# Optimization experiments

Hardware: AMD Instinct MI355X
Metric: run time of the kernel (lower is better)

Reference implementation:

```python
import jax, jax.numpy as jnp
import numpy as np

D_MODEL = 512
N_HEADS = 8
HEAD_SIZE = 64


def setup_inputs() -> dict:
    key = jax.random.key(0)
    ks = jax.random.split(key, 6)
    B, T = 4, 2048
    x_q = jax.random.normal(ks[0], (B, T, D_MODEL), dtype=jnp.float32)
    s = 1.0 / np.sqrt(D_MODEL)
    # per-head q/k/v projection weights, stacked: [H, head_size, d_model]
    Wq = jax.random.normal(ks[1], (N_HEADS, HEAD_SIZE, D_MODEL), dtype=jnp.float32) * s
    Wk = jax.random.normal(ks[2], (N_HEADS, HEAD_SIZE, D_MODEL), dtype=jnp.float32) * s
    Wv = jax.random.normal(ks[3], (N_HEADS, HEAD_SIZE, D_MODEL), dtype=jnp.float32) * s
    Wp = jax.random.normal(ks[4], (D_MODEL, D_MODEL), dtype=jnp.float32) * s
    bp = jax.random.normal(ks[5], (D_MODEL,), dtype=jnp.float32) * 0.01
    return {"x_q": x_q, "Wq": Wq, "Wk": Wk, "Wv": Wv, "Wp": Wp, "bp": bp}


def reference(x_q, Wq, Wk, Wv, Wp, bp):
    B, T, C = x_q.shape  # C == d_model
    # per-head projections: [B, H, T, K]
    q = jnp.einsum('btd,hkd->bhtk', x_q, Wq)
    k = jnp.einsum('btd,hkd->bhtk', x_q, Wk)
    v = jnp.einsum('btd,hkd->bhtk', x_q, Wv)
    # NOTE: original scales by C**-0.5 with C = d_model (not head_size)
    scores = jnp.einsum('bhtk,bhsk->bhts', q, k) * (C ** -0.5)
    causal = jnp.tril(jnp.ones((T, T), dtype=bool))
    scores = jnp.where(causal, scores, -jnp.inf)
    wei = jax.nn.softmax(scores, axis=-1)  # dropout is identity in eval
    out = jnp.einsum('bhts,bhsk->bhtk', wei, v)
    # concat heads: [B, T, H*K] == [B, T, d_model]
    out = out.transpose(0, 2, 1, 3).reshape(B, T, C)
    return out @ Wp.T + bp
```

## Files before the change

kernel.cpp:

```cpp
#include <hip/hip_runtime.h>
#include <hip/hip_bf16.h>

using bf16x8 = __attribute__((ext_vector_type(8))) __bf16;
using f32x4  = __attribute__((ext_vector_type(4))) float;
using f32x16 = __attribute__((ext_vector_type(16))) float;
using i32x4  = __attribute__((ext_vector_type(4))) int;

#define MFMA_16x16x32(a, b, c) __builtin_amdgcn_mfma_f32_16x16x32_bf16((a), (b), (c), 0, 0, 0)
#define MFMA32(a, b, c)        __builtin_amdgcn_mfma_f32_32x32x16_bf16((a), (b), (c), 0, 0, 0)

#define GLOAD16(g, l)                                                         \
    __builtin_amdgcn_global_load_lds(                                         \
        (const __attribute__((address_space(1))) unsigned int*)(g),           \
        (__attribute__((address_space(3))) unsigned int*)(l), 16, 0, 0)

__device__ __forceinline__ ushort f2bf(float f) {
    return __builtin_bit_cast(ushort, (__bf16)f);
}
__device__ __forceinline__ unsigned pk_bf16(float lo, float hi) {
    unsigned r;
    asm volatile("v_cvt_pk_bf16_f32 %0, %1, %2" : "=v"(r) : "v"(lo), "v"(hi));
    return r;
}
__device__ __forceinline__ void pl32_swap(unsigned &a, unsigned &b) {
    asm volatile("v_permlane32_swap_b32 %0, %1" : "+v"(a), "+v"(b));
}

__global__ __launch_bounds__(256) void cvt_bf16(
    const float* __restrict__ in, ushort* __restrict__ out, int n)
{
    const int i = (blockIdx.x * 256 + threadIdx.x) * 8;
    if (i + 8 <= n) {
        const f32x4 a = *(const f32x4*)(in + i);
        const f32x4 b = *(const f32x4*)(in + i + 4);
        union { ushort u[8]; i32x4 w; } p;
        #pragma unroll
        for (int j = 0; j < 4; ++j) { p.u[j] = f2bf(a[j]); p.u[4 + j] = f2bf(b[j]); }
        *(i32x4*)(out + i) = p.w;
    }
}

__global__ __launch_bounds__(256) void cvt_w3(
    const float* __restrict__ w0, const float* __restrict__ w1,
    const float* __restrict__ w2, ushort* __restrict__ out)
{
    const int i = (blockIdx.x * 256 + threadIdx.x) * 8;
    const int w = i >> 18, off = i & 262143;
    const float* src = (w == 0) ? w0 : ((w == 1) ? w1 : w2);
    const f32x4 a = *(const f32x4*)(src + off);
    const f32x4 b = *(const f32x4*)(src + off + 4);
    union { ushort u[8]; i32x4 v; } p;
    #pragma unroll
    for (int j = 0; j < 4; ++j) { p.u[j] = f2bf(a[j]); p.u[4 + j] = f2bf(b[j]); }
    *(i32x4*)(out + i) = p.v;
}

__global__ __launch_bounds__(256) void gemm_qkv3(
    const ushort* __restrict__ A, const ushort* __restrict__ Wbf,
    float qscale, ushort* __restrict__ qb, ushort* __restrict__ kb,
    ushort* __restrict__ vb)
{
    __shared__ ushort lA[2][128][32];
    __shared__ ushort lB[2][128][32];
    const int wsel = blockIdx.y >> 2;
    const int n0 = (blockIdx.y & 3) * 128;
    const ushort* W = Wbf + wsel * 262144;
    ushort* out = (wsel == 0) ? qb : ((wsel == 1) ? kb : vb);
    const float scale = (wsel == 0) ? qscale : 1.0f;

    const int m0 = blockIdx.x * 128;
    const int tid  = threadIdx.x;
    const int lane = tid & 63;
    const int wave = tid >> 6;
    const int wr = (wave >> 1) * 64, wc = (wave & 1) * 64;
    const int frow = lane & 15;
    const int fkp  = (((lane >> 4) ^ ((lane >> 1) & 3))) * 8;

    const int srw  = lane >> 2;
    const int scol = ((lane & 3) ^ ((lane >> 3) & 3)) * 8;

    f32x4 acc[4][4] = {};
    auto stage = [&](int k0, int b) {
        #pragma unroll
        for (int i = 0; i < 2; ++i) {
            const int rb = (wave * 2 + i) * 16;
            GLOAD16(A + (size_t)(m0 + rb + srw) * 512 + k0 + scol, &lA[b][rb][0]);
            GLOAD16(W + (size_t)(n0 + rb + srw) * 512 + k0 + scol, &lB[b][rb][0]);
        }
    };

    stage(0, 0);
    for (int t = 0; t < 16; ++t) {
        const int p = t & 1;
        __syncthreads();
        if (t + 1 < 16) stage((t + 1) * 32, p ^ 1);

        bf16x8 af[4], bg[4];
        #pragma unroll
        for (int m = 0; m < 4; ++m) af[m] = *(const bf16x8*)&lA[p][wr + m * 16 + frow][fkp];
        #pragma unroll
        for (int n = 0; n < 4; ++n) bg[n] = *(const bf16x8*)&lB[p][wc + n * 16 + frow][fkp];
        #pragma unroll
        for (int m = 0; m < 4; ++m)
            #pragma unroll
            for (int n = 0; n < 4; ++n)
                acc[m][n] = MFMA_16x16x32(af[m], bg[n], acc[m][n]);
    }

    const int rbase = (lane >> 4) * 4;
    const int ccol  = lane & 15;
    if (wsel == 2) {
        #pragma unroll
        for (int m = 0; m < 4; ++m)
            #pragma unroll
            for (int n = 0; n < 4; ++n) {
                const int col = n0 + wc + n * 16 + ccol;
                const int row0 = m0 + wr + m * 16 + rbase;
                unsigned long long u = 0;
                #pragma unroll
                for (int r = 0; r < 4; ++r)
                    u |= ((unsigned long long)f2bf(acc[m][n][r])) << (16 * r);
                const size_t idx = ((size_t)((row0 >> 11) * 8 + (col >> 6)) * 64
                                    + (col & 63)) * 2048 + (row0 & 2047);
                *(unsigned long long*)(out + idx) = u;
            }
    } else {
        #pragma unroll
        for (int m = 0; m < 4; ++m)
            #pragma unroll
            for (int n = 0; n < 4; ++n) {
                const int col = n0 + wc + n * 16 + ccol;
                #pragma unroll
                for (int r = 0; r < 4; ++r) {
                    const int row = m0 + wr + m * 16 + rbase + r;
                    out[(((row >> 11) * 8 + (col >> 6)) * 2048 + (row & 2047)) * 64 + (col & 63)]
                        = f2bf(acc[m][n][r] * scale);
                }
            }
    }
}

__global__ __launch_bounds__(256) void gemm_out(
    const ushort* __restrict__ A, const ushort* __restrict__ W,
    const float* __restrict__ bias, float* __restrict__ out)
{
    __shared__ ushort lA[2][128][32];
    __shared__ ushort lB[2][128][32];
    const int m0 = blockIdx.x * 128;
    const int n0 = blockIdx.y * 128;
    const int tid  = threadIdx.x;
    const int lane = tid & 63;
    const int wave = tid >> 6;
    const int wr = (wave >> 1) * 64, wc = (wave & 1) * 64;
    const int frow = lane & 15;
    const int fkp  = (((lane >> 4) ^ ((lane >> 1) & 3))) * 8;

    const int srw  = lane >> 2;
    const int scol = ((lane & 3) ^ ((lane >> 3) & 3)) * 8;

    f32x4 acc[4][4] = {};
    auto stage = [&](int k0, int b) {
        #pragma unroll
        for (int i = 0; i < 2; ++i) {
            const int rb = (wave * 2 + i) * 16;
            const int row = m0 + rb + srw, c = k0 + scol;
            const size_t ia = (((size_t)(row >> 11) * 8 + (c >> 6)) * 2048
                               + (row & 2047)) * 64 + (c & 63);
            GLOAD16(A + ia, &lA[b][rb][0]);
            GLOAD16(W + (size_t)(n0 + rb + srw) * 512 + k0 + scol, &lB[b][rb][0]);
        }
    };

    stage(0, 0);
    for (int t = 0; t < 16; ++t) {
        const int p = t & 1;
        __syncthreads();
        if (t + 1 < 16) stage((t + 1) * 32, p ^ 1);

        bf16x8 af[4], bg[4];
        #pragma unroll
        for (int m = 0; m < 4; ++m) af[m] = *(const bf16x8*)&lA[p][wr + m * 16 + frow][fkp];
        #pragma unroll
        for (int n = 0; n < 4; ++n) bg[n] = *(const bf16x8*)&lB[p][wc + n * 16 + frow][fkp];
        #pragma unroll
        for (int m = 0; m < 4; ++m)
            #pragma unroll
            for (int n = 0; n < 4; ++n)
                acc[m][n] = MFMA_16x16x32(af[m], bg[n], acc[m][n]);
    }

    const int rbase = (lane >> 4) * 4;
    const int ccol  = lane & 15;
    #pragma unroll
    for (int m = 0; m < 4; ++m)
        #pragma unroll
        for (int n = 0; n < 4; ++n) {
            const int col = n0 + wc + n * 16 + ccol;
            const float bv = bias[col];
            #pragma unroll
            for (int r = 0; r < 4; ++r) {
                const int row = m0 + wr + m * 16 + rbase + r;
                out[row * 512 + col] = acc[m][n][r] + bv;
            }
        }
}

__global__ __launch_bounds__(256, 2) void attn_kernel(
    const ushort* __restrict__ q, const ushort* __restrict__ k,
    const ushort* __restrict__ vt, ushort* __restrict__ att)
{
    __shared__ ushort lK[2][2][64][64];
    __shared__ ushort lV[2][2][64][64];

    const int NB   = (int)(gridDim.x * gridDim.y);
    const int NH   = NB >> 4;
    const int half = NB >> 1;
    const int n    = (int)(blockIdx.y * gridDim.x + blockIdx.x);
    const int r    = (n < half) ? n : (NB - 1 - (n - half));
    const int qt0  = (15 - r / NH) * 128;
    const int bh   = r % NH;

    const ushort* Q  = q  + (size_t)bh * 2048 * 64;
    const ushort* K  = k  + (size_t)bh * 2048 * 64;
    const ushort* VT = vt + (size_t)bh * 2048 * 64;
    ushort* O = att + (size_t)bh * 2048 * 64;

    const int tid = threadIdx.x;
    const int wv  = tid >> 6;
    const int l   = tid & 63;
    const int ql  = l & 31;
    const int hi  = l >> 5;
    const int wrow0 = qt0 + wv * 32;
    const int qrow  = wrow0 + ql;
    const int wmax  = wrow0 + 31;
    const int qkey  = ql & 7;
    const float LOG2E = 1.44269504088896f;

    const int srow = tid >> 2;
    const int sg   = (tid & 3) * 2;
    const int skey = srow & 7;

    bf16x8 aq[4];
    #pragma unroll
    for (int kk = 0; kk < 4; ++kk)
        aq[kk] = *(const bf16x8*)(Q + (size_t)qrow * 64 + kk * 16 + hi * 8);

    f32x16 o0 = {}, o1 = {};
    float mrun = -30000.0f, lrun = 0.0f;
    const int nt2 = qt0 / 128 + 1;

    i32x4 kr[2][2], vr[2][2];
    auto loadG = [&](int s0) {
        #pragma unroll
        for (int hf = 0; hf < 2; ++hf) {
            const ushort* kp = K + (size_t)(s0 + hf * 64 + srow) * 64 + (tid & 3) * 16;
            kr[hf][0] = *(const i32x4*)(kp);
            kr[hf][1] = *(const i32x4*)(kp + 8);
            const ushort* vp = VT + (size_t)srow * 2048 + s0 + hf * 64 + (tid & 3) * 16;
            vr[hf][0] = *(const i32x4*)(vp);
            vr[hf][1] = *(const i32x4*)(vp + 8);
        }
    };
    auto writeL = [&](int b) {
        #pragma unroll
        for (int hf = 0; hf < 2; ++hf) {
            *(i32x4*)&lK[b][hf][srow][((sg    ) ^ skey) * 8] = kr[hf][0];
            *(i32x4*)&lK[b][hf][srow][((sg + 1) ^ skey) * 8] = kr[hf][1];
            *(i32x4*)&lV[b][hf][srow][((sg    ) ^ skey) * 8] = vr[hf][0];
            *(i32x4*)&lV[b][hf][srow][((sg + 1) ^ skey) * 8] = vr[hf][1];
        }
    };

    loadG(0);
    writeL(0);
    if (nt2 > 1) loadG(128);

    for (int T = 0; T < nt2; ++T) {
        const int p  = T & 1;
        const int s0 = T * 128;
        __syncthreads();
        if (T + 1 < nt2) writeL(p ^ 1);
        if (T + 2 < nt2) loadG(s0 + 256);

        #pragma unroll
        for (int hf = 0; hf < 2; ++hf) {
            const int ss = s0 + hf * 64;
            if (ss > wmax) continue;

            f32x16 sa = {}, sb = {};
            #pragma unroll
            for (int kk = 0; kk < 4; ++kk) {
                const bf16x8 kb0 = *(const bf16x8*)&lK[p][hf][ql]     [((2 * kk + hi) ^ qkey) * 8];
                const bf16x8 kb1 = *(const bf16x8*)&lK[p][hf][32 + ql][((2 * kk + hi) ^ qkey) * 8];
                sa = MFMA32(kb0, aq[kk], sa);
                sb = MFMA32(kb1, aq[kk], sb);
            }

            if (ss + 63 > wrow0) {
                #pragma unroll
                for (int rr = 0; rr < 16; ++rr) {
                    const int cr = (rr & 3) + 8 * (rr >> 2) + 4 * hi;
                    if (ss + cr > qrow)      sa[rr] = -30000.0f;
                    if (ss + 32 + cr > qrow) sb[rr] = -30000.0f;
                }
            }

            float tm[16];
            #pragma unroll
            for (int rr = 0; rr < 16; ++rr) tm[rr] = fmaxf(sa[rr], sb[rr]);
            #pragma unroll
            for (int s = 8; s > 0; s >>= 1)
                #pragma unroll
                for (int rr = 0; rr < s; ++rr) tm[rr] = fmaxf(tm[rr], tm[rr + s]);
            float pmax = fmaxf(tm[0], __shfl_xor(tm[0], 32));

            if (__any(pmax > mrun + 8.0f)) {
                const float mnew  = fmaxf(mrun, pmax);
                const float alpha = exp2f((mrun - mnew) * LOG2E);
                mrun = mnew;
                lrun *= alpha;
                #pragma unroll
                for (int rr = 0; rr < 16; ++rr) {
                    const float ar = __shfl(alpha, (rr & 3) + 8 * (rr >> 2) + 4 * hi);
                    o0[rr] *= ar; o1[rr] *= ar;
                }
            }

            const float mb = mrun * LOG2E;
            #pragma unroll
            for (int rr = 0; rr < 16; ++rr) {
                sa[rr] = exp2f(fmaf(sa[rr], LOG2E, -mb));
                sb[rr] = exp2f(fmaf(sb[rr], LOG2E, -mb));
            }
            float tu[16];
            #pragma unroll
            for (int rr = 0; rr < 16; ++rr) tu[rr] = sa[rr] + sb[rr];
            #pragma unroll
            for (int s = 8; s > 0; s >>= 1)
                #pragma unroll
                for (int rr = 0; rr < s; ++rr) tu[rr] += tu[rr + s];
            lrun += tu[0] + __shfl_xor(tu[0], 32);

            unsigned paw[4][4];
            #pragma unroll
            for (int ks = 0; ks < 4; ++ks) {
                const int e = 2 * ks, f = 2 * ks + 1;
                const int ra = 4 * (e & 3), rb = 4 * (f & 3);
                unsigned A0, A1, B0, B1;
                if (e >> 2) { A0 = pk_bf16(sb[ra], sb[ra + 1]); A1 = pk_bf16(sb[ra + 2], sb[ra + 3]); }
                else        { A0 = pk_bf16(sa[ra], sa[ra + 1]); A1 = pk_bf16(sa[ra + 2], sa[ra + 3]); }
                if (f >> 2) { B0 = pk_bf16(sb[rb], sb[rb + 1]); B1 = pk_bf16(sb[rb + 2], sb[rb + 3]); }
                else        { B0 = pk_bf16(sa[rb], sa[rb + 1]); B1 = pk_bf16(sa[rb + 2], sa[rb + 3]); }
                pl32_swap(A0, B0);
                pl32_swap(A1, B1);
                paw[ks][0] = A0; paw[ks][1] = A1; paw[ks][2] = B0; paw[ks][3] = B1;
            }

            #pragma unroll
            for (int ks = 0; ks < 4; ++ks) {
                union { unsigned w[4]; bf16x8 v; } u;
                u.w[0] = paw[ks][0]; u.w[1] = paw[ks][1];
                u.w[2] = paw[ks][2]; u.w[3] = paw[ks][3];
                const bf16x8 v0 = *(const bf16x8*)&lV[p][hf][ql]     [((2 * ks + hi) ^ qkey) * 8];
                const bf16x8 v1 = *(const bf16x8*)&lV[p][hf][32 + ql][((2 * ks + hi) ^ qkey) * 8];
                o0 = MFMA32(u.v, v0, o0);
                o1 = MFMA32(u.v, v1, o1);
            }
        }
    }

    const float linv = 1.0f / fmaxf(lrun, 1e-30f);
    #pragma unroll
    for (int rr = 0; rr < 16; ++rr) {
        const int cr = (rr & 3) + 8 * (rr >> 2) + 4 * hi;
        const float li = __shfl(linv, cr);
        const int row = wrow0 + cr;
        O[(size_t)row * 64 + ql]      = f2bf(o0[rr] * li);
        O[(size_t)row * 64 + 32 + ql] = f2bf(o1[rr] * li);
    }
}

extern "C" void kernel_launch(void* const* d_in, const int* in_sizes, int n_in,
                              void* d_out, int out_size, void* d_ws, size_t ws_size,
                              hipStream_t stream) {
    const float* x  = (const float*)d_in[0];
    const float* Wq = (const float*)d_in[1];
    const float* Wk = (const float*)d_in[2];
    const float* Wv = (const float*)d_in[3];
    const float* Wp = (const float*)d_in[4];
    const float* bp = (const float*)d_in[5];
    float* out = (float*)d_out;

    const size_t NEL  = 4u * 8u * 2048u * 64u;
    const size_t NELB = 8u * 2048u * 64u;
    const float qscale = 0.04419417382415922f;

    if (ws_size >= 3u * NEL * sizeof(ushort)) {
        ushort* xbf  = (ushort*)d_out;
        ushort* qb   = xbf + NEL;
        ushort* kb   = (ushort*)d_ws;
        ushort* vb   = kb + NEL;
        ushort* ab   = vb + NEL;
        ushort* wbf  = ab;
        ushort* wpbf = kb;
        hipLaunchKernelGGL(cvt_bf16, dim3((int)(NEL / (256 * 8))), dim3(256), 0, stream,
                           x, xbf, (int)NEL);
        hipLaunchKernelGGL(cvt_w3, dim3(384), dim3(256), 0, stream, Wq, Wk, Wv, wbf);
        hipLaunchKernelGGL(gemm_qkv3, dim3(64, 12), dim3(256), 0, stream,
                           xbf, wbf, qscale, qb, kb, vb);
        hipLaunchKernelGGL(attn_kernel, dim3(16, 32), dim3(256), 0, stream, qb, kb, vb, ab);
        hipLaunchKernelGGL(cvt_bf16, dim3(128), dim3(256), 0, stream, Wp, wpbf, 262144);
        hipLaunchKernelGGL(gemm_out, dim3(64, 4), dim3(256), 0, stream, ab, wpbf, bp, out);
    } else {
        ushort* kb  = (ushort*)d_ws;
        ushort* vb  = kb + NELB;
        ushort* ab  = vb + NELB;
        ushort* wbf = ab;
        for (int b = 0; b < 4; ++b) {
            const float* xb = x + (size_t)b * 2048u * 512u;
            float* ob = out + (size_t)b * 2048u * 512u;
            ushort* xbf  = (ushort*)ob;
            ushort* qb   = xbf + NELB;
            ushort* wpbf = kb;
            hipLaunchKernelGGL(cvt_bf16, dim3((int)(NELB / (256 * 8))), dim3(256), 0, stream,
                               xb, xbf, (int)NELB);
            hipLaunchKernelGGL(cvt_w3, dim3(384), dim3(256), 0, stream, Wq, Wk, Wv, wbf);
            hipLaunchKernelGGL(gemm_qkv3, dim3(16, 12), dim3(256), 0, stream,
                               xbf, wbf, qscale, qb, kb, vb);
            hipLaunchKernelGGL(attn_kernel, dim3(16, 8), dim3(256), 0, stream, qb, kb, vb, ab);
            hipLaunchKernelGGL(cvt_bf16, dim3(128), dim3(256), 0, stream, Wp, wpbf, 262144);
            hipLaunchKernelGGL(gemm_out, dim3(16, 4), dim3(256), 0, stream, ab, wpbf, bp, ob);
        }
    }
}
```

Before: 99.20 us.

## Merge conversion kernels and process 128-key tile with single softmax update

The x and Wq/Wk/Wv fp32-to-bf16 conversions are merged into one launch, so one kernel launch and its gap go away. In the attention loop, both 64-key halves of each 128-key tile are now scored together, and a single max/rescale/sum pass covers all of them instead of one per half. This halves the online-softmax bookkeeping and the cross-lane reductions, and exposes more independent MFMA work. The cost is higher register pressure from holding four score accumulators at once, which may lower occupancy.

```diff
diff --git a/kernel.cpp b/kernel.cpp
--- a/kernel.cpp
+++ b/kernel.cpp
@@ -40,19 +40,33 @@
     }
 }
 
-__global__ __launch_bounds__(256) void cvt_w3(
+__global__ __launch_bounds__(256) void cvt_fused(
+    const float* __restrict__ x, ushort* __restrict__ xbf, int nx, int nxb,
     const float* __restrict__ w0, const float* __restrict__ w1,
-    const float* __restrict__ w2, ushort* __restrict__ out)
+    const float* __restrict__ w2, ushort* __restrict__ wbf)
 {
-    const int i = (blockIdx.x * 256 + threadIdx.x) * 8;
-    const int w = i >> 18, off = i & 262143;
-    const float* src = (w == 0) ? w0 : ((w == 1) ? w1 : w2);
-    const f32x4 a = *(const f32x4*)(src + off);
-    const f32x4 b = *(const f32x4*)(src + off + 4);
-    union { ushort u[8]; i32x4 v; } p;
-    #pragma unroll
-    for (int j = 0; j < 4; ++j) { p.u[j] = f2bf(a[j]); p.u[4 + j] = f2bf(b[j]); }
-    *(i32x4*)(out + i) = p.v;
+    const int b = (int)blockIdx.x;
+    if (b < nxb) {
+        const int i = (b * 256 + (int)threadIdx.x) * 8;
+        if (i + 8 <= nx) {
+            const f32x4 a = *(const f32x4*)(x + i);
+            const f32x4 c = *(const f32x4*)(x + i + 4);
+            union { ushort u[8]; i32x4 w; } p;
+            #pragma unroll
+            for (int j = 0; j < 4; ++j) { p.u[j] = f2bf(a[j]); p.u[4 + j] = f2bf(c[j]); }
+            *(i32x4*)(xbf + i) = p.w;
+        }
+    } else {
+        const int i = ((b - nxb) * 256 + (int)threadIdx.x) * 8;
+        const int w = i >> 18, off = i & 262143;
+        const float* src = (w == 0) ? w0 : ((w == 1) ? w1 : w2);
+        const f32x4 a = *(const f32x4*)(src + off);
+        const f32x4 c = *(const f32x4*)(src + off + 4);
+        union { ushort u[8]; i32x4 v; } p;
+        #pragma unroll
+        for (int j = 0; j < 4; ++j) { p.u[j] = f2bf(a[j]); p.u[4 + j] = f2bf(c[j]); }
+        *(i32x4*)(wbf + i) = p.v;
+    }
 }
 
 __global__ __launch_bounds__(256) void gemm_qkv3(
@@ -282,87 +296,144 @@
         if (T + 1 < nt2) writeL(p ^ 1);
         if (T + 2 < nt2) loadG(s0 + 256);
 
-        #pragma unroll
-        for (int hf = 0; hf < 2; ++hf) {
-            const int ss = s0 + hf * 64;
-            if (ss > wmax) continue;
-
-            f32x16 sa = {}, sb = {};
+        const bool act1 = (s0 + 64 <= wmax);
+
+        f32x16 sa0 = {}, sb0 = {}, sa1 = {}, sb1 = {};
+        #pragma unroll
+        for (int kk = 0; kk < 4; ++kk) {
+            const bf16x8 a0 = *(const bf16x8*)&lK[p][0][ql]     [((2 * kk + hi) ^ qkey) * 8];
+            const bf16x8 b0 = *(const bf16x8*)&lK[p][0][32 + ql][((2 * kk + hi) ^ qkey) * 8];
+            sa0 = MFMA32(a0, aq[kk], sa0);
+            sb0 = MFMA32(b0, aq[kk], sb0);
+        }
+        if (act1) {
             #pragma unroll
             for (int kk = 0; kk < 4; ++kk) {
-                const bf16x8 kb0 = *(const bf16x8*)&lK[p][hf][ql]     [((2 * kk + hi) ^ qkey) * 8];
-                const bf16x8 kb1 = *(const bf16x8*)&lK[p][hf][32 + ql][((2 * kk + hi) ^ qkey) * 8];
-                sa = MFMA32(kb0, aq[kk], sa);
-                sb = MFMA32(kb1, aq[kk], sb);
-            }
-
-            if (ss + 63 > wrow0) {
-                #pragma unroll
-                for (int rr = 0; rr < 16; ++rr) {
-                    const int cr = (rr & 3) + 8 * (rr >> 2) + 4 * hi;
-                    if (ss + cr > qrow)      sa[rr] = -30000.0f;
-                    if (ss + 32 + cr > qrow) sb[rr] = -30000.0f;
-                }
-            }
-
-            float tm[16];
-            #pragma unroll
-            for (int rr = 0; rr < 16; ++rr) tm[rr] = fmaxf(sa[rr], sb[rr]);
-            #pragma unroll
-            for (int s = 8; s > 0; s >>= 1)
-                #pragma unroll
-                for (int rr = 0; rr < s; ++rr) tm[rr] = fmaxf(tm[rr], tm[rr + s]);
-            float pmax = fmaxf(tm[0], __shfl_xor(tm[0], 32));
-
-            if (__any(pmax > mrun + 8.0f)) {
-                const float mnew  = fmaxf(mrun, pmax);
-                const float alpha = exp2f((mrun - mnew) * LOG2E);
-                mrun = mnew;
-                lrun *= alpha;
-                #pragma unroll
-                for (int rr = 0; rr < 16; ++rr) {
-                    const float ar = __shfl(alpha, (rr & 3) + 8 * (rr >> 2) + 4 * hi);
-                    o0[rr] *= ar; o1[rr] *= ar;
-                }
-            }
-
-            const float mb = mrun * LOG2E;
+                const bf16x8 a1 = *(const bf16x8*)&lK[p][1][ql]     [((2 * kk + hi) ^ qkey) * 8];
+                const bf16x8 b1 = *(const bf16x8*)&lK[p][1][32 + ql][((2 * kk + hi) ^ qkey) * 8];
+                sa1 = MFMA32(a1, aq[kk], sa1);
+                sb1 = MFMA32(b1, aq[kk], sb1);
+            }
+        }
+
+        if (s0 + 63 > wrow0) {
             #pragma unroll
             for (int rr = 0; rr < 16; ++rr) {
-                sa[rr] = exp2f(fmaf(sa[rr], LOG2E, -mb));
-                sb[rr] = exp2f(fmaf(sb[rr], LOG2E, -mb));
-            }
-            float tu[16];
-            #pragma unroll
-            for (int rr = 0; rr < 16; ++rr) tu[rr] = sa[rr] + sb[rr];
-            #pragma unroll
-            for (int s = 8; s > 0; s >>= 1)
-                #pragma unroll
-                for (int rr = 0; rr < s; ++rr) tu[rr] += tu[rr + s];
-            lrun += tu[0] + __shfl_xor(tu[0], 32);
-
+                const int cr = (rr & 3) + 8 * (rr >> 2) + 4 * hi;
+                if (s0 + cr > qrow)      sa0[rr] = -30000.0f;
+                if (s0 + 32 + cr > qrow) sb0[rr] = -30000.0f;
+            }
+        }
+        if (act1 && (s0 + 127 > wrow0)) {
+            #pragma unroll
+            for (int rr = 0; rr < 16; ++rr) {
+                const int cr = (rr & 3) + 8 * (rr >> 2) + 4 * hi;
+                if (s0 + 64 + cr > qrow) sa1[rr] = -30000.0f;
+                if (s0 + 96 + cr > qrow) sb1[rr] = -30000.0f;
+            }
+        }
+
+        float tm[16];
+        #pragma unroll
+        for (int rr = 0; rr < 16; ++rr) tm[rr] = fmaxf(sa0[rr], sb0[rr]);
+        if (act1) {
+            #pragma unroll
+            for (int rr = 0; rr < 16; ++rr)
+                tm[rr] = fmaxf(tm[rr], fmaxf(sa1[rr], sb1[rr]));
+        }
+        #pragma unroll
+        for (int s = 8; s > 0; s >>= 1)
+            #pragma unroll
+            for (int rr = 0; rr < s; ++rr) tm[rr] = fmaxf(tm[rr], tm[rr + s]);
+        float pmax = fmaxf(tm[0], __shfl_xor(tm[0], 32));
+
+        if (__any(pmax > mrun + 8.0f)) {
+            const float mnew  = fmaxf(mrun, pmax);
+            const float alpha = exp2f((mrun - mnew) * LOG2E);
+            mrun = mnew;
+            lrun *= alpha;
+            #pragma unroll
+            for (int rr = 0; rr < 16; ++rr) {
+                const float ar = __shfl(alpha, (rr & 3) + 8 * (rr >> 2) + 4 * hi);
+                o0[rr] *= ar; o1[rr] *= ar;
+            }
+        }
+
+        const float mb = mrun * LOG2E;
+        #pragma unroll
+        for (int rr = 0; rr < 16; ++rr) {
+            sa0[rr] = exp2f(fmaf(sa0[rr], LOG2E, -mb));
+            sb0[rr] = exp2f(fmaf(sb0[rr], LOG2E, -mb));
+        }
+        if (act1) {
+            #pragma unroll
+            for (int rr = 0; rr < 16; ++rr) {
+                sa1[rr] = exp2f(fmaf(sa1[rr], LOG2E, -mb));
+                sb1[rr] = exp2f(fmaf(sb1[rr], LOG2E, -mb));
+            }
+        }
+
+        float tu[16];
+        #pragma unroll
+        for (int rr = 0; rr < 16; ++rr) tu[rr] = sa0[rr] + sb0[rr];
+        if (act1) {
+            #pragma unroll
+            for (int rr = 0; rr < 16; ++rr) tu[rr] += sa1[rr] + sb1[rr];
+        }
+        #pragma unroll
+        for (int s = 8; s > 0; s >>= 1)
+            #pragma unroll
+            for (int rr = 0; rr < s; ++rr) tu[rr] += tu[rr + s];
+        lrun += tu[0] + __shfl_xor(tu[0], 32);
+
+        {
             unsigned paw[4][4];
             #pragma unroll
             for (int ks = 0; ks < 4; ++ks) {
                 const int e = 2 * ks, f = 2 * ks + 1;
                 const int ra = 4 * (e & 3), rb = 4 * (f & 3);
                 unsigned A0, A1, B0, B1;
-                if (e >> 2) { A0 = pk_bf16(sb[ra], sb[ra + 1]); A1 = pk_bf16(sb[ra + 2], sb[ra + 3]); }
-                else        { A0 = pk_bf16(sa[ra], sa[ra + 1]); A1 = pk_bf16(sa[ra + 2], sa[ra + 3]); }
-                if (f >> 2) { B0 = pk_bf16(sb[rb], sb[rb + 1]); B1 = pk_bf16(sb[rb + 2], sb[rb + 3]); }
-                else        { B0 = pk_bf16(sa[rb], sa[rb + 1]); B1 = pk_bf16(sa[rb + 2], sa[rb + 3]); }
+                if (e >> 2) { A0 = pk_bf16(sb0[ra], sb0[ra + 1]); A1 = pk_bf16(sb0[ra + 2], sb0[ra + 3]); }
+                else        { A0 = pk_bf16(sa0[ra], sa0[ra + 1]); A1 = pk_bf16(sa0[ra + 2], sa0[ra + 3]); }
+                if (f >> 2) { B0 = pk_bf16(sb0[rb], sb0[rb + 1]); B1 = pk_bf16(sb0[rb + 2], sb0[rb + 3]); }
+                else        { B0 = pk_bf16(sa0[rb], sa0[rb + 1]); B1 = pk_bf16(sa0[rb + 2], sa0[rb + 3]); }
                 pl32_swap(A0, B0);
                 pl32_swap(A1, B1);
                 paw[ks][0] = A0; paw[ks][1] = A1; paw[ks][2] = B0; paw[ks][3] = B1;
             }
-
             #pragma unroll
             for (int ks = 0; ks < 4; ++ks) {
                 union { unsigned w[4]; bf16x8 v; } u;
                 u.w[0] = paw[ks][0]; u.w[1] = paw[ks][1];
                 u.w[2] = paw[ks][2]; u.w[3] = paw[ks][3];
-                const bf16x8 v0 = *(const bf16x8*)&lV[p][hf][ql]     [((2 * ks + hi) ^ qkey) * 8];
-                const bf16x8 v1 = *(const bf16x8*)&lV[p][hf][32 + ql][((2 * ks + hi) ^ qkey) * 8];
+                const bf16x8 v0 = *(const bf16x8*)&lV[p][0][ql]     [((2 * ks + hi) ^ qkey) * 8];
+                const bf16x8 v1 = *(const bf16x8*)&lV[p][0][32 + ql][((2 * ks + hi) ^ qkey) * 8];
+                o0 = MFMA32(u.v, v0, o0);
+                o1 = MFMA32(u.v, v1, o1);
+            }
+        }
+        if (act1) {
+            unsigned paw[4][4];
+            #pragma unroll
+            for (int ks = 0; ks < 4; ++ks) {
+                const int e = 2 * ks, f = 2 * ks + 1;
+                const int ra = 4 * (e & 3), rb = 4 * (f & 3);
+                unsigned A0, A1, B0, B1;
+                if (e >> 2) { A0 = pk_bf16(sb1[ra], sb1[ra + 1]); A1 = pk_bf16(sb1[ra + 2], sb1[ra + 3]); }
+                else        { A0 = pk_bf16(sa1[ra], sa1[ra + 1]); A1 = pk_bf16(sa1[ra + 2], sa1[ra + 3]); }
+                if (f >> 2) { B0 = pk_bf16(sb1[rb], sb1[rb + 1]); B1 = pk_bf16(sb1[rb + 2], sb1[rb + 3]); }
+                else        { B0 = pk_bf16(sa1[rb], sa1[rb + 1]); B1 = pk_bf16(sa1[rb + 2], sa1[rb + 3]); }
+                pl32_swap(A0, B0);
+                pl32_swap(A1, B1);
+                paw[ks][0] = A0; paw[ks][1] = A1; paw[ks][2] = B0; paw[ks][3] = B1;
+            }
+            #pragma unroll
+            for (int ks = 0; ks < 4; ++ks) {
+                union { unsigned w[4]; bf16x8 v; } u;
+                u.w[0] = paw[ks][0]; u.w[1] = paw[ks][1];
+                u.w[2] = paw[ks][2]; u.w[3] = paw[ks][3];
+                const bf16x8 v0 = *(const bf16x8*)&lV[p][1][ql]     [((2 * ks + hi) ^ qkey) * 8];
+                const bf16x8 v1 = *(const bf16x8*)&lV[p][1][32 + ql][((2 * ks + hi) ^ qkey) * 8];
                 o0 = MFMA32(u.v, v0, o0);
                 o1 = MFMA32(u.v, v1, o1);
             }
@@ -403,9 +474,8 @@
         ushort* ab   = vb + NEL;
         ushort* wbf  = ab;
         ushort* wpbf = kb;
-        hipLaunchKernelGGL(cvt_bf16, dim3((int)(NEL / (256 * 8))), dim3(256), 0, stream,
-                           x, xbf, (int)NEL);
-        hipLaunchKernelGGL(cvt_w3, dim3(384), dim3(256), 0, stream, Wq, Wk, Wv, wbf);
+        hipLaunchKernelGGL(cvt_fused, dim3((int)(NEL / (256 * 8)) + 384), dim3(256), 0, stream,
+                           x, xbf, (int)NEL, (int)(NEL / (256 * 8)), Wq, Wk, Wv, wbf);
         hipLaunchKernelGGL(gemm_qkv3, dim3(64, 12), dim3(256), 0, stream,
                            xbf, wbf, qscale, qb, kb, vb);
         hipLaunchKernelGGL(attn_kernel, dim3(16, 32), dim3(256), 0, stream, qb, kb, vb, ab);
@@ -422,9 +492,8 @@
             ushort* xbf  = (ushort*)ob;
             ushort* qb   = xbf + NELB;
             ushort* wpbf = kb;
-            hipLaunchKernelGGL(cvt_bf16, dim3((int)(NELB / (256 * 8))), dim3(256), 0, stream,
-                               xb, xbf, (int)NELB);
-            hipLaunchKernelGGL(cvt_w3, dim3(384), dim3(256), 0, stream, Wq, Wk, Wv, wbf);
+            hipLaunchKernelGGL(cvt_fused, dim3((int)(NELB / (256 * 8)) + 384), dim3(256), 0, stream,
+                               xb, xbf, (int)NELB, (int)(NELB / (256 * 8)), Wq, Wk, Wv, wbf);
             hipLaunchKernelGGL(gemm_qkv3, dim3(16, 12), dim3(256), 0, stream,
                                xbf, wbf, qscale, qb, kb, vb);
             hipLaunchKernelGGL(attn_kernel, dim3(16, 8), dim3(256), 0, stream, qb, kb, vb, ab);
```

Result: faster. 94.21 us (-5.0%).
